# Performance work log

Measured on AMD Instinct MI355X. Metric: run time of the kernel, lower is better.

Reference implementation:

```python
import jax, jax.numpy as jnp
import numpy as np
from jax import lax

C = 64
EPS = 1e-5


def _layernorm_c(x, g, b):
    # LayerNorm over channel dim of NCHW tensor (matches nn.LayerNorm([C]) applied on NHWC)
    mu = jnp.mean(x, axis=1, keepdims=True)
    var = jnp.var(x, axis=1, keepdims=True)
    xn = (x - mu) * lax.rsqrt(var + EPS)
    return xn * g[None, :, None, None] + b[None, :, None, None]


def _conv1x1(x, w, b):
    # w: [O, I]
    return jnp.einsum('bihw,oi->bohw', x, w) + b[None, :, None, None]


def _dwconv3x3(x, w, b):
    # depthwise 3x3, w: [C, 3, 3]
    k = w[:, None, :, :]  # OIHW with I=1
    y = lax.conv_general_dilated(x, k, (1, 1), 'SAME',
                                 feature_group_count=w.shape[0],
                                 dimension_numbers=('NCHW', 'OIHW', 'NCHW'))
    return y + b[None, :, None, None]


def setup_inputs() -> dict:
    key = jax.random.key(0)
    ks = jax.random.split(key, 24)
    s = 0.02
    d = {}
    d['x'] = jax.random.normal(ks[0], (4, C, 64, 64), dtype=jnp.float32)
    # CTA params
    d['cta_ln_g'] = jnp.ones((C,), jnp.float32)
    d['cta_ln_b'] = jnp.zeros((C,), jnp.float32)
    d['q_w'] = jax.random.normal(ks[1], (C, C), jnp.float32) * s
    d['q_b'] = jnp.zeros((C,), jnp.float32)
    d['k_w'] = jax.random.normal(ks[2], (C, 3, 3), jnp.float32) * s
    d['k_b'] = jnp.zeros((C,), jnp.float32)
    d['v_w'] = jax.random.normal(ks[3], (C, 3, 3), jnp.float32) * s
    d['v_b'] = jnp.zeros((C,), jnp.float32)
    d['cta_out_w'] = jax.random.normal(ks[4], (C, C), jnp.float32) * s
    d['cta_out_b'] = jnp.zeros((C,), jnp.float32)
    # NLE params
    d['nle_ln_g'] = jnp.ones((C,), jnp.float32)
    d['nle_ln_b'] = jnp.zeros((C,), jnp.float32)
    d['b1_w1'] = jax.random.normal(ks[5], (2 * C, C), jnp.float32) * s
    d['b1_b1'] = jnp.zeros((2 * C,), jnp.float32)
    d['b1_w2'] = jax.random.normal(ks[6], (2 * C, 3, 3), jnp.float32) * s
    d['b1_b2'] = jnp.zeros((2 * C,), jnp.float32)
    d['b2_w1'] = jax.random.normal(ks[7], (2 * C, C), jnp.float32) * s
    d['b2_b1'] = jnp.zeros((2 * C,), jnp.float32)
    d['b2_w2'] = jax.random.normal(ks[8], (2 * C, 3, 3), jnp.float32) * s
    d['b2_b2'] = jnp.zeros((2 * C,), jnp.float32)
    d['nle_out_w'] = jax.random.normal(ks[9], (C, 2 * C), jnp.float32) * s
    d['nle_out_b'] = jnp.zeros((C,), jnp.float32)
    return d


def csam_forward(x, cta_ln_g, cta_ln_b, q_w, q_b, k_w, k_b, v_w, v_b, cta_out_w, cta_out_b,
                 nle_ln_g, nle_ln_b, b1_w1, b1_b1, b1_w2, b1_b2, b2_w1, b2_b1, b2_w2, b2_b2,
                 nle_out_w, nle_out_b):
    B, Cc, H, W = x.shape
    scale = jnp.sqrt(jnp.float32(Cc))
    # --- CTA ---
    xn = _layernorm_c(x, cta_ln_g, cta_ln_b)
    q = _conv1x1(xn, q_w, q_b).reshape(B, Cc, H * W)      # [B,C,N]
    k = _dwconv3x3(xn, k_w, k_b).reshape(B, Cc, H * W)    # [B,C,N]
    v = _dwconv3x3(xn, v_w, v_b).reshape(B, Cc, H * W)    # [B,C,N]
    attn = jnp.einsum('bcn,bcm->bnm', q, k) / scale        # [B,N,N]
    attn = jax.nn.softmax(attn, axis=-1)
    out = jnp.einsum('bnm,bcm->bcn', attn, v).reshape(B, Cc, H, W)
    x_att = _conv1x1(out, cta_out_w, cta_out_b) + x
    # --- NLE ---
    xn2 = _layernorm_c(x_att, nle_ln_g, nle_ln_b)
    br1 = jax.nn.gelu(_dwconv3x3(_conv1x1(xn2, b1_w1, b1_b1), b1_w2, b1_b2), approximate=False)
    br2 = jax.nn.gelu(_dwconv3x3(_conv1x1(xn2, b2_w1, b2_b1), b2_w2, b2_b2), approximate=False)
    nle = _conv1x1(br1 * br2, nle_out_w, nle_out_b)
    return nle + x_att


def reference(x, cta_ln_g, cta_ln_b, q_w, q_b, k_w, k_b, v_w, v_b, cta_out_w, cta_out_b,
              nle_ln_g, nle_ln_b, b1_w1, b1_b1, b1_w2, b1_b2, b2_w1, b2_b1, b2_w2, b2_b2,
              nle_out_w, nle_out_b):
    return csam_forward(x, cta_ln_g, cta_ln_b, q_w, q_b, k_w, k_b, v_w, v_b, cta_out_w, cta_out_b,
                        nle_ln_g, nle_ln_b, b1_w1, b1_b1, b1_w2, b1_b2, b2_w1, b2_b1, b2_w2, b2_b2,
                        nle_out_w, nle_out_b)
```

## Files before the change

kernel.cpp:

```cpp
#include <hip/hip_runtime.h>
#include <hip/hip_bf16.h>
#include <math.h>

#define NPIX 4096
#define CH 64
#define BATCH 4
#define NSPLIT 4

typedef __attribute__((ext_vector_type(8))) short short8;
typedef __attribute__((ext_vector_type(4))) float f32x4;
typedef __attribute__((ext_vector_type(4))) unsigned short us4;
typedef __attribute__((ext_vector_type(4))) unsigned int u32x4;

static __device__ __forceinline__ unsigned short f2bf(float f) {
  union { float f; unsigned u; } v; v.f = f;
  unsigned u = v.u;
  unsigned r = u + 0x7FFF + ((u >> 16) & 1);
  return (unsigned short)(r >> 16);
}
static __device__ __forceinline__ float bf2f(unsigned short u) {
  union { unsigned u; float f; } v; v.u = ((unsigned)u) << 16; return v.f;
}
static __device__ __forceinline__ unsigned cvtpk(float lo, float hi) {
  unsigned r;
  asm("v_cvt_pk_bf16_f32 %0, %1, %2" : "=v"(r) : "v"(lo), "v"(hi));
  return r;
}

__global__ __launch_bounds__(256) void k_ln_q(
    const float* __restrict__ x, const float* __restrict__ lg, const float* __restrict__ lb,
    const float* __restrict__ qw, const float* __restrict__ qb,
    float* __restrict__ xn, unsigned short* __restrict__ Q)
{
  __shared__ float xT[64][64];
  __shared__ unsigned short xB[64][64];
  int tid = threadIdx.x, px = tid & 63, g4 = tid >> 6;
  int idx0 = blockIdx.x * 64;
  int idx = idx0 + px;
  int b = idx >> 12, p = idx & 4095;
  const float* xb = x + (size_t)b * CH * NPIX + p;
  for (int j = 0; j < 16; ++j) { int c = 16 * g4 + j; xT[c][px] = xb[(size_t)c * NPIX]; }
  __syncthreads();
  float xv[64]; float s = 0.f;
#pragma unroll
  for (int c = 0; c < 64; ++c) { xv[c] = xT[c][px]; s += xv[c]; }
  float mu = s * (1.f / 64.f), vs = 0.f;
#pragma unroll
  for (int c = 0; c < 64; ++c) { float d = xv[c] - mu; vs += d * d; }
  float rs = rsqrtf(vs * (1.f / 64.f) + 1e-5f);
#pragma unroll
  for (int c = 0; c < 64; ++c) xv[c] = (xv[c] - mu) * rs * lg[c] + lb[c];

  float* xnb = xn + (size_t)b * CH * NPIX + p;
#define LNQ_WR(C0)                                                             \
  {                                                                            \
    unsigned short t[16];                                                      \
    _Pragma("unroll") for (int j = 0; j < 16; ++j) {                           \
      float v = xv[C0 + j];                                                    \
      xnb[(size_t)(C0 + j) * NPIX] = v;                                        \
      t[j] = f2bf(v);                                                          \
    }                                                                          \
    *(short8*)&xB[px][(((C0 / 8) + 0) ^ (px & 7)) * 8] = *(short8*)t;          \
    *(short8*)&xB[px][(((C0 / 8) + 1) ^ (px & 7)) * 8] = *(short8*)(t + 8);    \
  }
  if (g4 == 0) LNQ_WR(0)
  else if (g4 == 1) LNQ_WR(16)
  else if (g4 == 2) LNQ_WR(32)
  else LNQ_WR(48)
#undef LNQ_WR
  __syncthreads();

  int lane = tid & 63, l15 = lane & 15, gg = lane >> 4;
  short8 af[2];
#pragma unroll
  for (int kc = 0; kc < 2; ++kc) {
    const float* wp = qw + (size_t)(g4 * 16 + l15) * 64 + kc * 32 + 8 * gg;
    unsigned short t[8];
#pragma unroll
    for (int j = 0; j < 8; ++j) t[j] = f2bf(wp[j]);
    af[kc] = *(short8*)t;
  }
  float bv[4];
#pragma unroll
  for (int r = 0; r < 4; ++r) bv[r] = qb[g4 * 16 + 4 * gg + r];
#pragma unroll
  for (int ct = 0; ct < 4; ++ct) {
    f32x4 acc = {bv[0], bv[1], bv[2], bv[3]};
    int row = ct * 16 + l15;
    short8 bf0 = *(const short8*)&xB[row][((0 + gg) ^ (row & 7)) * 8];
    short8 bf1 = *(const short8*)&xB[row][((4 + gg) ^ (row & 7)) * 8];
    acc = __builtin_amdgcn_mfma_f32_16x16x32_bf16(af[0], bf0, acc, 0, 0, 0);
    acc = __builtin_amdgcn_mfma_f32_16x16x32_bf16(af[1], bf1, acc, 0, 0, 0);
    us4 v;
#pragma unroll
    for (int r = 0; r < 4; ++r) v[r] = f2bf(acc[r] * 0.125f);
    *(us4*)(Q + (size_t)(idx0 + row) * 64 + g4 * 16 + 4 * gg) = v;
  }
}

__global__ __launch_bounds__(256) void k_dwkv(
    const float* __restrict__ xn,
    const float* __restrict__ kw, const float* __restrict__ kb,
    const float* __restrict__ vw, const float* __restrict__ vb,
    unsigned short* __restrict__ K, unsigned short* __restrict__ VT)
{
  int idx = blockIdx.x * 256 + threadIdx.x;
  int b = idx >> 12, p = idx & 4095;
  int h = p >> 6, w = p & 63;
  int c0 = blockIdx.y * 8;
  size_t base = (size_t)b * CH * NPIX;
  unsigned short kq[8];
#pragma unroll
  for (int j = 0; j < 8; ++j) {
    int c = c0 + j;
    const float* xc = xn + base + (size_t)c * NPIX;
    float ka = kb[c], va = vb[c];
#pragma unroll
    for (int dy = -1; dy <= 1; ++dy) {
#pragma unroll
      for (int dx = -1; dx <= 1; ++dx) {
        int hh = h + dy, ww = w + dx;
        float xvv = (hh >= 0 && hh < 64 && ww >= 0 && ww < 64) ? xc[hh * 64 + ww] : 0.f;
        int t = (dy + 1) * 3 + (dx + 1);
        ka += kw[c * 9 + t] * xvv;
        va += vw[c * 9 + t] * xvv;
      }
    }
    kq[j] = f2bf(ka);
    VT[((size_t)b * CH + c) * NPIX + p] = f2bf(va);
  }
  *(short8*)(K + (size_t)idx * 64 + c0) = *(short8*)(kq);
}

__global__ __launch_bounds__(256) void k_attn(
    const unsigned short* __restrict__ Q, const unsigned short* __restrict__ K,
    const unsigned short* __restrict__ VT, unsigned short* __restrict__ OPb,
    float* __restrict__ LS)
{
  __shared__ float red[4][16][68];
  __shared__ float lsls[4][4][16];

  int tid = threadIdx.x;
  int wid = tid >> 6, lane = tid & 63;
  int l15 = lane & 15, g = lane >> 4;
  int b = blockIdx.y, split = blockIdx.z;
  int qbase = blockIdx.x * 64;

  const unsigned short* Qb = Q + (size_t)b * NPIX * CH;
  const unsigned short* Kb = K + (size_t)b * NPIX * CH;
  const unsigned short* Vb = VT + (size_t)b * CH * NPIX;

  short8 qf[4][2];
#pragma unroll
  for (int qt = 0; qt < 4; ++qt)
#pragma unroll
    for (int kc = 0; kc < 2; ++kc)
      qf[qt][kc] = *(const short8*)(Qb + (size_t)(qbase + qt * 16 + l15) * CH + kc * 32 + 8 * g);

  f32x4 acc[4][4];
#pragma unroll
  for (int qt = 0; qt < 4; ++qt)
#pragma unroll
    for (int cs = 0; cs < 4; ++cs) acc[qt][cs] = (f32x4){0.f, 0.f, 0.f, 0.f};
  float lsum[4] = {0.f, 0.f, 0.f, 0.f};

  int kperm = 8 * (l15 >> 2) + (l15 & 3);
  int kbase = split * 1024 + wid * 256;

  for (int s = 0; s < 8; ++s) {
    int key0 = kbase + s * 32;
    const unsigned short* kp = Kb + (size_t)(key0 + kperm) * CH + 8 * g;
    short8 kf00 = *(const short8*)(kp);
    short8 kf01 = *(const short8*)(kp + 32);
    short8 kf10 = *(const short8*)(kp + 4 * CH);
    short8 kf11 = *(const short8*)(kp + 4 * CH + 32);
    const unsigned short* vp = Vb + (size_t)l15 * NPIX + key0 + 8 * g;
    short8 vf0 = *(const short8*)(vp);
    short8 vf1 = *(const short8*)(vp + 16 * NPIX);
    short8 vf2 = *(const short8*)(vp + 32 * NPIX);
    short8 vf3 = *(const short8*)(vp + 48 * NPIX);

    __builtin_amdgcn_s_setprio(1);
#pragma unroll
    for (int qt = 0; qt < 4; ++qt) {
      f32x4 s0 = {0.f, 0.f, 0.f, 0.f}, s1 = {0.f, 0.f, 0.f, 0.f};
      s0 = __builtin_amdgcn_mfma_f32_16x16x32_bf16(kf00, qf[qt][0], s0, 0, 0, 0);
      s0 = __builtin_amdgcn_mfma_f32_16x16x32_bf16(kf01, qf[qt][1], s0, 0, 0, 0);
      s1 = __builtin_amdgcn_mfma_f32_16x16x32_bf16(kf10, qf[qt][0], s1, 0, 0, 0);
      s1 = __builtin_amdgcn_mfma_f32_16x16x32_bf16(kf11, qf[qt][1], s1, 0, 0, 0);
      float p0 = __expf(s0[0]), p1 = __expf(s0[1]), p2 = __expf(s0[2]), p3 = __expf(s0[3]);
      float p4 = __expf(s1[0]), p5 = __expf(s1[1]), p6 = __expf(s1[2]), p7 = __expf(s1[3]);
      lsum[qt] += (p0 + p1) + (p2 + p3) + (p4 + p5) + (p6 + p7);
      u32x4 pk;
      pk[0] = cvtpk(p0, p1); pk[1] = cvtpk(p2, p3);
      pk[2] = cvtpk(p4, p5); pk[3] = cvtpk(p6, p7);
      short8 pb = *(short8*)&pk;
      acc[qt][0] = __builtin_amdgcn_mfma_f32_16x16x32_bf16(vf0, pb, acc[qt][0], 0, 0, 0);
      acc[qt][1] = __builtin_amdgcn_mfma_f32_16x16x32_bf16(vf1, pb, acc[qt][1], 0, 0, 0);
      acc[qt][2] = __builtin_amdgcn_mfma_f32_16x16x32_bf16(vf2, pb, acc[qt][2], 0, 0, 0);
      acc[qt][3] = __builtin_amdgcn_mfma_f32_16x16x32_bf16(vf3, pb, acc[qt][3], 0, 0, 0);
    }
    __builtin_amdgcn_s_setprio(0);
  }

#pragma unroll
  for (int qt = 0; qt < 4; ++qt) {
    lsum[qt] += __shfl_xor(lsum[qt], 16, 64);
    lsum[qt] += __shfl_xor(lsum[qt], 32, 64);
  }
  if (g == 0) {
#pragma unroll
    for (int qt = 0; qt < 4; ++qt) lsls[wid][qt][l15] = lsum[qt];
  }

  size_t sb = ((size_t)split * BATCH + b) * NPIX;
#pragma unroll
  for (int qt = 0; qt < 4; ++qt) {
    __syncthreads();
#pragma unroll
    for (int cs = 0; cs < 4; ++cs)
      *(f32x4*)&red[wid][l15][cs * 16 + 4 * g] = acc[qt][cs];
    __syncthreads();
    int q = tid >> 4, ch = (tid & 15) * 4;
    f32x4 v = *(f32x4*)&red[0][q][ch];
    v += *(f32x4*)&red[1][q][ch];
    v += *(f32x4*)&red[2][q][ch];
    v += *(f32x4*)&red[3][q][ch];
    us4 o4;
#pragma unroll
    for (int i = 0; i < 4; ++i) o4[i] = f2bf(v[i]);
    *(us4*)(OPb + (sb + qbase + qt * 16 + q) * 64 + ch) = o4;
  }
  __syncthreads();
  if (tid < 64) {
    int qt = tid >> 4, q = tid & 15;
    LS[sb + qbase + qt * 16 + q] =
        lsls[0][qt][q] + lsls[1][qt][q] + lsls[2][qt][q] + lsls[3][qt][q];
  }
}

__global__ __launch_bounds__(256) void k_reduce(
    const unsigned short* __restrict__ OPb, const float* __restrict__ LSv,
    unsigned short* __restrict__ AOT)
{
  int tid = threadIdx.x;
  size_t e0 = (size_t)blockIdx.x * 4096;
#pragma unroll
  for (int h = 0; h < 2; ++h) {
    int off = (h * 256 + tid) * 8;
    int pix = blockIdx.x * 64 + (off >> 6);
    float sv[8] = {0.f, 0.f, 0.f, 0.f, 0.f, 0.f, 0.f, 0.f};
    float ls = 0.f;
#pragma unroll
    for (int sp = 0; sp < NSPLIT; ++sp) {
      short8 a = *(const short8*)(OPb + (size_t)sp * BATCH * NPIX * 64 + e0 + off);
#pragma unroll
      for (int j = 0; j < 8; ++j) sv[j] += bf2f((unsigned short)a[j]);
      ls += LSv[(size_t)sp * BATCH * NPIX + pix];
    }
    float inv = 1.f / ls;
    unsigned short t[8];
#pragma unroll
    for (int j = 0; j < 8; ++j) t[j] = f2bf(sv[j] * inv);
    *(short8*)(AOT + e0 + off) = *(short8*)t;
  }
}

__global__ __launch_bounds__(256) void k_proj_ln2(
    const unsigned short* __restrict__ AOT, const float* __restrict__ x,
    const float* __restrict__ ow, const float* __restrict__ ob,
    const float* __restrict__ lg, const float* __restrict__ lb,
    float* __restrict__ xatt, unsigned short* __restrict__ xn2T)
{
  __shared__ float sm1[4][4][16], sm2[4][4][16];
  int tid = threadIdx.x;
  int wid = tid >> 6, lane = tid & 63;
  int l15 = lane & 15, g = lane >> 4;
  int b = blockIdx.y, pxb = blockIdx.x * 64;
  const unsigned short* In = AOT + ((size_t)b * NPIX + pxb) * 64;

  short8 af[2];
#pragma unroll
  for (int kc = 0; kc < 2; ++kc) {
    const float* wp = ow + (size_t)(wid * 16 + l15) * 64 + kc * 32 + 8 * g;
    unsigned short t[8];
#pragma unroll
    for (int j = 0; j < 8; ++j) t[j] = f2bf(wp[j]);
    af[kc] = *(short8*)t;
  }
  float bv[4], lgv[4], lbv[4];
#pragma unroll
  for (int r = 0; r < 4; ++r) {
    int o = wid * 16 + 4 * g + r;
    bv[r] = ob[o]; lgv[r] = lg[o]; lbv[r] = lb[o];
  }
  f32x4 acc[4];
#pragma unroll
  for (int ct = 0; ct < 4; ++ct) acc[ct] = (f32x4){bv[0], bv[1], bv[2], bv[3]};
#pragma unroll
  for (int ct = 0; ct < 4; ++ct) {
    short8 bf0 = *(const short8*)(In + (size_t)(ct * 16 + l15) * 64 + 8 * g);
    short8 bf1 = *(const short8*)(In + (size_t)(ct * 16 + l15) * 64 + 32 + 8 * g);
    acc[ct] = __builtin_amdgcn_mfma_f32_16x16x32_bf16(af[0], bf0, acc[ct], 0, 0, 0);
    acc[ct] = __builtin_amdgcn_mfma_f32_16x16x32_bf16(af[1], bf1, acc[ct], 0, 0, 0);
  }

  float xo[4][4];
#pragma unroll
  for (int ct = 0; ct < 4; ++ct) {
    int p = pxb + ct * 16 + l15;
    float s1 = 0.f, s2 = 0.f;
#pragma unroll
    for (int r = 0; r < 4; ++r) {
      int o = wid * 16 + 4 * g + r;
      size_t oi = ((size_t)b * CH + o) * NPIX + p;
      float v = acc[ct][r] + x[oi];
      xatt[oi] = v;
      xo[ct][r] = v;
      s1 += v; s2 += v * v;
    }
    s1 += __shfl_xor(s1, 16, 64); s1 += __shfl_xor(s1, 32, 64);
    s2 += __shfl_xor(s2, 16, 64); s2 += __shfl_xor(s2, 32, 64);
    if (g == 0) { sm1[wid][ct][l15] = s1; sm2[wid][ct][l15] = s2; }
  }
  __syncthreads();
#pragma unroll
  for (int ct = 0; ct < 4; ++ct) {
    int p = pxb + ct * 16 + l15;
    float mu = (sm1[0][ct][l15] + sm1[1][ct][l15] + sm1[2][ct][l15] + sm1[3][ct][l15]) * (1.f / 64.f);
    float ms = (sm2[0][ct][l15] + sm2[1][ct][l15] + sm2[2][ct][l15] + sm2[3][ct][l15]) * (1.f / 64.f);
    float rs = rsqrtf(ms - mu * mu + 1e-5f);
    us4 v4;
#pragma unroll
    for (int r = 0; r < 4; ++r) v4[r] = f2bf((xo[ct][r] - mu) * rs * lgv[r] + lbv[r]);
    *(us4*)(xn2T + ((size_t)b * NPIX + p) * 64 + wid * 16 + 4 * g) = v4;
  }
}

__global__ __launch_bounds__(256) void k_pw_both(
    const unsigned short* __restrict__ xn2T,
    const float* __restrict__ w1, const float* __restrict__ bb1,
    const float* __restrict__ w2, const float* __restrict__ bb2,
    float* __restrict__ t1, float* __restrict__ t2)
{
  int tid = threadIdx.x;
  int wid = tid >> 6, lane = tid & 63;
  int l15 = lane & 15, g = lane >> 4;
  int b = blockIdx.y, pxb = blockIdx.x * 64;
  const unsigned short* In = xn2T + ((size_t)b * NPIX + pxb) * 64;
  const float* W  = (wid & 2) ? w2 : w1;
  const float* bb = (wid & 2) ? bb2 : bb1;
  float* t        = (wid & 2) ? t2 : t1;
  int oh = (wid & 1) * 64;

  short8 af[4][2];
#pragma unroll
  for (int ot = 0; ot < 4; ++ot)
#pragma unroll
    for (int kc = 0; kc < 2; ++kc) {
      const float* wp = W + (size_t)(oh + ot * 16 + l15) * 64 + kc * 32 + 8 * g;
      unsigned short tt[8];
#pragma unroll
      for (int j = 0; j < 8; ++j) tt[j] = f2bf(wp[j]);
      af[ot][kc] = *(short8*)tt;
    }
  f32x4 acc[4][4];
#pragma unroll
  for (int ot = 0; ot < 4; ++ot) {
    float b0 = bb[oh + ot * 16 + 4 * g + 0];
    float b1 = bb[oh + ot * 16 + 4 * g + 1];
    float b2 = bb[oh + ot * 16 + 4 * g + 2];
    float b3 = bb[oh + ot * 16 + 4 * g + 3];
#pragma unroll
    for (int ct = 0; ct < 4; ++ct) acc[ot][ct] = (f32x4){b0, b1, b2, b3};
  }
#pragma unroll
  for (int ct = 0; ct < 4; ++ct) {
    short8 bf0 = *(const short8*)(In + (size_t)(ct * 16 + l15) * 64 + 8 * g);
    short8 bf1 = *(const short8*)(In + (size_t)(ct * 16 + l15) * 64 + 32 + 8 * g);
#pragma unroll
    for (int ot = 0; ot < 4; ++ot) {
      acc[ot][ct] = __builtin_amdgcn_mfma_f32_16x16x32_bf16(af[ot][0], bf0, acc[ot][ct], 0, 0, 0);
      acc[ot][ct] = __builtin_amdgcn_mfma_f32_16x16x32_bf16(af[ot][1], bf1, acc[ot][ct], 0, 0, 0);
    }
  }
#pragma unroll
  for (int ot = 0; ot < 4; ++ot)
#pragma unroll
    for (int ct = 0; ct < 4; ++ct) {
      int p = pxb + ct * 16 + l15;
#pragma unroll
      for (int r = 0; r < 4; ++r) {
        int o = oh + ot * 16 + 4 * g + r;
        t[((size_t)b * 128 + o) * NPIX + p] = acc[ot][ct][r];
      }
    }
}

__global__ __launch_bounds__(256) void k_dwgelu(
    const float* __restrict__ t1, const float* __restrict__ t2,
    const float* __restrict__ w1, const float* __restrict__ bb1,
    const float* __restrict__ w2, const float* __restrict__ bb2,
    unsigned short* __restrict__ g12T)
{
  int idx = blockIdx.x * 256 + threadIdx.x;
  int b = idx >> 12, p = idx & 4095;
  int h = p >> 6, w = p & 63;
  int c0 = blockIdx.y * 8;
  unsigned short outv[8];
#pragma unroll
  for (int j = 0; j < 8; ++j) {
    int c = c0 + j;
    size_t tb = ((size_t)b * 128 + c) * NPIX;
    float a1 = bb1[c], a2 = bb2[c];
#pragma unroll
    for (int dy = -1; dy <= 1; ++dy) {
#pragma unroll
      for (int dx = -1; dx <= 1; ++dx) {
        int hh = h + dy, ww = w + dx;
        bool ok = (hh >= 0 && hh < 64 && ww >= 0 && ww < 64);
        float v1 = ok ? t1[tb + hh * 64 + ww] : 0.f;
        float v2 = ok ? t2[tb + hh * 64 + ww] : 0.f;
        int t = (dy + 1) * 3 + (dx + 1);
        a1 += w1[c * 9 + t] * v1;
        a2 += w2[c * 9 + t] * v2;
      }
    }
    float ge1 = 0.5f * a1 * (1.f + erff(a1 * 0.70710678118654752f));
    float ge2 = 0.5f * a2 * (1.f + erff(a2 * 0.70710678118654752f));
    outv[j] = f2bf(ge1 * ge2);
  }
  *(short8*)(g12T + (size_t)idx * 128 + c0) = *(short8*)outv;
}

__global__ __launch_bounds__(256) void k_out(
    const float* __restrict__ W, const float* __restrict__ bias,
    const unsigned short* __restrict__ InT, const float* __restrict__ res,
    float* __restrict__ outF)
{
  int tid = threadIdx.x;
  int wid = tid >> 6, lane = tid & 63;
  int l15 = lane & 15, g = lane >> 4;
  int b = blockIdx.y, pxb = blockIdx.x * 64;
  const unsigned short* In = InT + ((size_t)b * NPIX + pxb) * 128;

  short8 af[4];
#pragma unroll
  for (int kc = 0; kc < 4; ++kc) {
    const float* wp = W + (size_t)(wid * 16 + l15) * 128 + kc * 32 + 8 * g;
    unsigned short t[8];
#pragma unroll
    for (int j = 0; j < 8; ++j) t[j] = f2bf(wp[j]);
    af[kc] = *(short8*)t;
  }
  float bv[4];
#pragma unroll
  for (int r = 0; r < 4; ++r) bv[r] = bias[wid * 16 + 4 * g + r];
#pragma unroll
  for (int ct = 0; ct < 4; ++ct) {
    f32x4 acc = {bv[0], bv[1], bv[2], bv[3]};
#pragma unroll
    for (int kc = 0; kc < 4; ++kc) {
      short8 bf = *(const short8*)(In + (size_t)(ct * 16 + l15) * 128 + kc * 32 + 8 * g);
      acc = __builtin_amdgcn_mfma_f32_16x16x32_bf16(af[kc], bf, acc, 0, 0, 0);
    }
    int p = pxb + ct * 16 + l15;
#pragma unroll
    for (int r = 0; r < 4; ++r) {
      int o = wid * 16 + 4 * g + r;
      size_t oi = ((size_t)b * CH + o) * NPIX + p;
      outF[oi] = acc[r] + res[oi];
    }
  }
}

extern "C" void kernel_launch(void* const* d_in, const int* in_sizes, int n_in,
                              void* d_out, int out_size, void* d_ws, size_t ws_size,
                              hipStream_t stream) {
  const float* x        = (const float*)d_in[0];
  const float* cta_ln_g = (const float*)d_in[1];
  const float* cta_ln_b = (const float*)d_in[2];
  const float* q_w      = (const float*)d_in[3];
  const float* q_b      = (const float*)d_in[4];
  const float* k_w      = (const float*)d_in[5];
  const float* k_b      = (const float*)d_in[6];
  const float* v_w      = (const float*)d_in[7];
  const float* v_b      = (const float*)d_in[8];
  const float* cta_out_w= (const float*)d_in[9];
  const float* cta_out_b= (const float*)d_in[10];
  const float* nle_ln_g = (const float*)d_in[11];
  const float* nle_ln_b = (const float*)d_in[12];
  const float* b1_w1    = (const float*)d_in[13];
  const float* b1_b1    = (const float*)d_in[14];
  const float* b1_w2    = (const float*)d_in[15];
  const float* b1_b2    = (const float*)d_in[16];
  const float* b2_w1    = (const float*)d_in[17];
  const float* b2_b1    = (const float*)d_in[18];
  const float* b2_w2    = (const float*)d_in[19];
  const float* b2_b2    = (const float*)d_in[20];
  const float* nle_out_w= (const float*)d_in[21];
  const float* nle_out_b= (const float*)d_in[22];

  char* ws = (char*)d_ws;
  float*          xn   = (float*)(ws);
  unsigned short* Qb   = (unsigned short*)(ws + (4u  << 20));
  unsigned short* Kb   = (unsigned short*)(ws + (6u  << 20));
  unsigned short* VTb  = (unsigned short*)(ws + (8u  << 20));
  unsigned short* OPb  = (unsigned short*)(ws + (10u << 20));
  float*          LSb  = (float*)(ws + (18u << 20));
  unsigned short* AOT  = (unsigned short*)(ws + (19u << 20));
  float*          xatt = (float*)(ws + (21u << 20));
  unsigned short* xn2T = (unsigned short*)(ws + (25u << 20));
  float*          t1   = (float*)(ws + (27u << 20));
  float*          t2   = (float*)(ws + (35u << 20));
  unsigned short* g12T = (unsigned short*)(ws);

  k_ln_q     <<<256, 256, 0, stream>>>(x, cta_ln_g, cta_ln_b, q_w, q_b, xn, Qb);
  k_dwkv     <<<dim3(64, 8), 256, 0, stream>>>(xn, k_w, k_b, v_w, v_b, Kb, VTb);
  k_attn     <<<dim3(64, BATCH, NSPLIT), 256, 0, stream>>>(Qb, Kb, VTb, OPb, LSb);
  k_reduce   <<<256, 256, 0, stream>>>(OPb, LSb, AOT);
  k_proj_ln2 <<<dim3(64, 4), 256, 0, stream>>>(AOT, x, cta_out_w, cta_out_b, nle_ln_g, nle_ln_b, xatt, xn2T);
  k_pw_both  <<<dim3(64, 4), 256, 0, stream>>>(xn2T, b1_w1, b1_b1, b2_w1, b2_b1, t1, t2);
  k_dwgelu   <<<dim3(64, 16), 256, 0, stream>>>(t1, t2, b1_w2, b1_b2, b2_w2, b2_b2, g12T);
  k_out      <<<dim3(64, 4), 256, 0, stream>>>(nle_out_w, nle_out_b, g12T, xatt, (float*)d_out);
}
```

Measured before the change: 87.48 us.

## Restructure attention kernel to stage K/V tiles in double-buffered swizzled LDS

The attention kernel now gives each wave its own 16 queries and iterates over all 1024 keys of its split. K and V tiles are staged cooperatively into double-buffered, XOR-swizzled shared memory, with register prefetch of the next tile. Before, each wave covered 64 queries and a quarter of the keys, loading K/V straight from global memory and reducing partial outputs across waves through LDS. The aim is to remove the cross-wave reduction and the repeated global loads. The cost is a P round-trip through LDS to reshape the MFMA operand, a __syncthreads per tile, and scalar 16-bit output stores.

```diff
diff --git a/kernel.cpp b/kernel.cpp
--- a/kernel.cpp
+++ b/kernel.cpp
@@ -20,11 +20,6 @@
 }
 static __device__ __forceinline__ float bf2f(unsigned short u) {
   union { unsigned u; float f; } v; v.u = ((unsigned)u) << 16; return v.f;
-}
-static __device__ __forceinline__ unsigned cvtpk(float lo, float hi) {
-  unsigned r;
-  asm("v_cvt_pk_bf16_f32 %0, %1, %2" : "=v"(r) : "v"(lo), "v"(hi));
-  return r;
 }
 
 __global__ __launch_bounds__(256) void k_ln_q(
@@ -132,110 +127,130 @@
   *(short8*)(K + (size_t)idx * 64 + c0) = *(short8*)(kq);
 }
 
-__global__ __launch_bounds__(256) void k_attn(
+__global__ __launch_bounds__(256, 4) void k_attn(
     const unsigned short* __restrict__ Q, const unsigned short* __restrict__ K,
     const unsigned short* __restrict__ VT, unsigned short* __restrict__ OPb,
     float* __restrict__ LS)
 {
-  __shared__ float red[4][16][68];
-  __shared__ float lsls[4][4][16];
+  __shared__ unsigned short kls[2][64][64];
+  __shared__ unsigned short vls[2][64][64];
+  __shared__ unsigned short plds[4][16][64];
 
   int tid = threadIdx.x;
-  int wid = tid >> 6, lane = tid & 63;
+  int wid = tid >> 6;
+  int lane = tid & 63;
   int l15 = lane & 15, g = lane >> 4;
-  int b = blockIdx.y, split = blockIdx.z;
-  int qbase = blockIdx.x * 64;
+  int b = blockIdx.y;
+  int split = blockIdx.z;
+  int nbase = blockIdx.x * 64 + wid * 16;
 
   const unsigned short* Qb = Q + (size_t)b * NPIX * CH;
   const unsigned short* Kb = K + (size_t)b * NPIX * CH;
   const unsigned short* Vb = VT + (size_t)b * CH * NPIX;
 
-  short8 qf[4][2];
-#pragma unroll
-  for (int qt = 0; qt < 4; ++qt)
-#pragma unroll
-    for (int kc = 0; kc < 2; ++kc)
-      qf[qt][kc] = *(const short8*)(Qb + (size_t)(qbase + qt * 16 + l15) * CH + kc * 32 + 8 * g);
-
-  f32x4 acc[4][4];
-#pragma unroll
-  for (int qt = 0; qt < 4; ++qt)
-#pragma unroll
-    for (int cs = 0; cs < 4; ++cs) acc[qt][cs] = (f32x4){0.f, 0.f, 0.f, 0.f};
+  short8 qf0 = *(const short8*)(Qb + (size_t)(nbase + l15) * CH + 8 * g);
+  short8 qf1 = *(const short8*)(Qb + (size_t)(nbase + l15) * CH + 32 + 8 * g);
+
+  f32x4 oacc[4];
+#pragma unroll
+  for (int i = 0; i < 4; ++i) oacc[i] = (f32x4){0.f, 0.f, 0.f, 0.f};
   float lsum[4] = {0.f, 0.f, 0.f, 0.f};
-
-  int kperm = 8 * (l15 >> 2) + (l15 & 3);
-  int kbase = split * 1024 + wid * 256;
-
-  for (int s = 0; s < 8; ++s) {
-    int key0 = kbase + s * 32;
-    const unsigned short* kp = Kb + (size_t)(key0 + kperm) * CH + 8 * g;
-    short8 kf00 = *(const short8*)(kp);
-    short8 kf01 = *(const short8*)(kp + 32);
-    short8 kf10 = *(const short8*)(kp + 4 * CH);
-    short8 kf11 = *(const short8*)(kp + 4 * CH + 32);
-    const unsigned short* vp = Vb + (size_t)l15 * NPIX + key0 + 8 * g;
-    short8 vf0 = *(const short8*)(vp);
-    short8 vf1 = *(const short8*)(vp + 16 * NPIX);
-    short8 vf2 = *(const short8*)(vp + 32 * NPIX);
-    short8 vf3 = *(const short8*)(vp + 48 * NPIX);
-
-    __builtin_amdgcn_s_setprio(1);
-#pragma unroll
-    for (int qt = 0; qt < 4; ++qt) {
-      f32x4 s0 = {0.f, 0.f, 0.f, 0.f}, s1 = {0.f, 0.f, 0.f, 0.f};
-      s0 = __builtin_amdgcn_mfma_f32_16x16x32_bf16(kf00, qf[qt][0], s0, 0, 0, 0);
-      s0 = __builtin_amdgcn_mfma_f32_16x16x32_bf16(kf01, qf[qt][1], s0, 0, 0, 0);
-      s1 = __builtin_amdgcn_mfma_f32_16x16x32_bf16(kf10, qf[qt][0], s1, 0, 0, 0);
-      s1 = __builtin_amdgcn_mfma_f32_16x16x32_bf16(kf11, qf[qt][1], s1, 0, 0, 0);
-      float p0 = __expf(s0[0]), p1 = __expf(s0[1]), p2 = __expf(s0[2]), p3 = __expf(s0[3]);
-      float p4 = __expf(s1[0]), p5 = __expf(s1[1]), p6 = __expf(s1[2]), p7 = __expf(s1[3]);
-      lsum[qt] += (p0 + p1) + (p2 + p3) + (p4 + p5) + (p6 + p7);
-      u32x4 pk;
-      pk[0] = cvtpk(p0, p1); pk[1] = cvtpk(p2, p3);
-      pk[2] = cvtpk(p4, p5); pk[3] = cvtpk(p6, p7);
-      short8 pb = *(short8*)&pk;
-      acc[qt][0] = __builtin_amdgcn_mfma_f32_16x16x32_bf16(vf0, pb, acc[qt][0], 0, 0, 0);
-      acc[qt][1] = __builtin_amdgcn_mfma_f32_16x16x32_bf16(vf1, pb, acc[qt][1], 0, 0, 0);
-      acc[qt][2] = __builtin_amdgcn_mfma_f32_16x16x32_bf16(vf2, pb, acc[qt][2], 0, 0, 0);
-      acc[qt][3] = __builtin_amdgcn_mfma_f32_16x16x32_bf16(vf3, pb, acc[qt][3], 0, 0, 0);
-    }
-    __builtin_amdgcn_s_setprio(0);
-  }
-
-#pragma unroll
-  for (int qt = 0; qt < 4; ++qt) {
-    lsum[qt] += __shfl_xor(lsum[qt], 16, 64);
-    lsum[qt] += __shfl_xor(lsum[qt], 32, 64);
-  }
-  if (g == 0) {
-#pragma unroll
-    for (int qt = 0; qt < 4; ++qt) lsls[wid][qt][l15] = lsum[qt];
+  unsigned short* pwv = &plds[wid][0][0];
+
+  int srow = tid >> 3, sch = tid & 7;
+  int wa0 = srow * 64 + ((sch ^ (srow & 7)) * 8);
+  int srow1 = srow + 32;
+  int wa1 = srow1 * 64 + ((sch ^ (srow1 & 7)) * 8);
+  const unsigned short* ksrc0 = Kb + (size_t)(split * 1024 + srow) * CH + sch * 8;
+  const unsigned short* ksrc1 = Kb + (size_t)(split * 1024 + srow1) * CH + sch * 8;
+  const unsigned short* vsrc0 = Vb + (size_t)srow * NPIX + split * 1024 + sch * 8;
+  const unsigned short* vsrc1 = Vb + (size_t)srow1 * NPIX + split * 1024 + sch * 8;
+
+  short8 kg0, kg1, vg0, vg1;
+  kg0 = *(const short8*)(ksrc0);
+  kg1 = *(const short8*)(ksrc1);
+  vg0 = *(const short8*)(vsrc0);
+  vg1 = *(const short8*)(vsrc1);
+  *(short8*)(&kls[0][0][0] + wa0) = kg0;
+  *(short8*)(&kls[0][0][0] + wa1) = kg1;
+  *(short8*)(&vls[0][0][0] + wa0) = vg0;
+  *(short8*)(&vls[0][0][0] + wa1) = vg1;
+  __syncthreads();
+
+  for (int t = 0; t < 16; ++t) {
+    if (t < 15) {
+      int ko = (t + 1) * 64;
+      kg0 = *(const short8*)(ksrc0 + (size_t)ko * CH);
+      kg1 = *(const short8*)(ksrc1 + (size_t)ko * CH);
+      vg0 = *(const short8*)(vsrc0 + ko);
+      vg1 = *(const short8*)(vsrc1 + ko);
+    }
+
+    const unsigned short* kb = &kls[t & 1][0][0];
+    const unsigned short* vb = &vls[t & 1][0][0];
+
+    f32x4 s[4];
+#pragma unroll
+    for (int cb = 0; cb < 4; ++cb) {
+      int row = cb * 16 + l15;
+      short8 kf0 = *(const short8*)(kb + row * 64 + (((0 + g) ^ (row & 7)) * 8));
+      short8 kf1 = *(const short8*)(kb + row * 64 + (((4 + g) ^ (row & 7)) * 8));
+      f32x4 acc = {0.f, 0.f, 0.f, 0.f};
+      acc = __builtin_amdgcn_mfma_f32_16x16x32_bf16(qf0, kf0, acc, 0, 0, 0);
+      acc = __builtin_amdgcn_mfma_f32_16x16x32_bf16(qf1, kf1, acc, 0, 0, 0);
+      s[cb] = acc;
+    }
+
+#pragma unroll
+    for (int cb = 0; cb < 4; ++cb) {
+#pragma unroll
+      for (int r = 0; r < 4; ++r) {
+        float p = __expf(s[cb][r]);
+        lsum[r] += p;
+        int row = 4 * g + r;
+        int key = cb * 16 + l15;
+        pwv[row * 64 + (((key >> 3) ^ (row & 7)) * 8) + (key & 7)] = f2bf(p);
+      }
+    }
+    short8 pf0 = *(const short8*)(pwv + l15 * 64 + (((0 + g) ^ (l15 & 7)) * 8));
+    short8 pf1 = *(const short8*)(pwv + l15 * 64 + (((4 + g) ^ (l15 & 7)) * 8));
+
+#pragma unroll
+    for (int cs = 0; cs < 4; ++cs) {
+      int row = cs * 16 + l15;
+      short8 vf0 = *(const short8*)(vb + row * 64 + (((0 + g) ^ (row & 7)) * 8));
+      short8 vf1 = *(const short8*)(vb + row * 64 + (((4 + g) ^ (row & 7)) * 8));
+      oacc[cs] = __builtin_amdgcn_mfma_f32_16x16x32_bf16(pf0, vf0, oacc[cs], 0, 0, 0);
+      oacc[cs] = __builtin_amdgcn_mfma_f32_16x16x32_bf16(pf1, vf1, oacc[cs], 0, 0, 0);
+    }
+
+    if (t < 15) {
+      unsigned short* kw_ = &kls[(t + 1) & 1][0][0];
+      unsigned short* vw_ = &vls[(t + 1) & 1][0][0];
+      *(short8*)(kw_ + wa0) = kg0;
+      *(short8*)(kw_ + wa1) = kg1;
+      *(short8*)(vw_ + wa0) = vg0;
+      *(short8*)(vw_ + wa1) = vg1;
+    }
+    __syncthreads();
+  }
+
+#pragma unroll
+  for (int m = 1; m <= 8; m <<= 1) {
+#pragma unroll
+    for (int r = 0; r < 4; ++r) lsum[r] += __shfl_xor(lsum[r], m, 64);
   }
 
   size_t sb = ((size_t)split * BATCH + b) * NPIX;
-#pragma unroll
-  for (int qt = 0; qt < 4; ++qt) {
-    __syncthreads();
-#pragma unroll
-    for (int cs = 0; cs < 4; ++cs)
-      *(f32x4*)&red[wid][l15][cs * 16 + 4 * g] = acc[qt][cs];
-    __syncthreads();
-    int q = tid >> 4, ch = (tid & 15) * 4;
-    f32x4 v = *(f32x4*)&red[0][q][ch];
-    v += *(f32x4*)&red[1][q][ch];
-    v += *(f32x4*)&red[2][q][ch];
-    v += *(f32x4*)&red[3][q][ch];
-    us4 o4;
-#pragma unroll
-    for (int i = 0; i < 4; ++i) o4[i] = f2bf(v[i]);
-    *(us4*)(OPb + (sb + qbase + qt * 16 + q) * 64 + ch) = o4;
-  }
-  __syncthreads();
-  if (tid < 64) {
-    int qt = tid >> 4, q = tid & 15;
-    LS[sb + qbase + qt * 16 + q] =
-        lsls[0][qt][q] + lsls[1][qt][q] + lsls[2][qt][q] + lsls[3][qt][q];
+  unsigned short* Ob = OPb + (sb + nbase) * CH;
+#pragma unroll
+  for (int r = 0; r < 4; ++r) {
+    int n = 4 * g + r;
+    Ob[n * CH +  0 + l15] = f2bf(oacc[0][r]);
+    Ob[n * CH + 16 + l15] = f2bf(oacc[1][r]);
+    Ob[n * CH + 32 + l15] = f2bf(oacc[2][r]);
+    Ob[n * CH + 48 + l15] = f2bf(oacc[3][r]);
+    if (l15 == 0) LS[sb + nbase + n] = lsum[r];
   }
 }
 
```

Result: faster. 80.53 us (-8.0%).
